# Optimization experiments

Hardware: AMD Instinct MI355X
Metric: run time of the kernel (lower is better)

Reference implementation:

```python
import jax, jax.numpy as jnp
import numpy as np

B, T, E, V, H = 4096, 80, 100, 10000, 64


def setup_inputs() -> dict:
    key = jax.random.key(0)
    ks = jax.random.split(key, 8)
    s = lambda k, sh: (jax.random.normal(k, sh, jnp.float32) * 0.05)
    return {
        "inputs": jax.random.randint(ks[0], (B, T), 0, V),
        "emb": s(ks[1], (V, E)),
        "Wx0": s(ks[2], (E, H)),
        "Wh0": s(ks[3], (H, H)),
        "b0": jnp.zeros((H,), jnp.float32),
        "Wx1": s(ks[4], (H, H)),
        "Wh1": s(ks[5], (H, H)),
        "b1": jnp.zeros((H,), jnp.float32),
        "Wf": s(ks[6], (H, 1)),
        "bf": jnp.zeros((1,), jnp.float32),
    }


def reference(inputs, emb, Wx0, Wh0, b0, Wx1, Wh1, b1, Wf, bf):
    # Embedding lookup: [B, T] int -> [B, T, E]
    x = emb[inputs]
    xT = jnp.swapaxes(x, 0, 1)  # [T, B, E] for scan over time

    def step(carry, xt):
        h0, h1 = carry
        # SimpleRNNCell layer 0: tanh(x@Wx + h@Wh + b)
        h0 = jnp.tanh(xt @ Wx0 + h0 @ Wh0 + b0)
        # SimpleRNNCell layer 1 consumes layer-0 output
        h1 = jnp.tanh(h0 @ Wx1 + h1 @ Wh1 + b1)
        return (h0, h1), None

    init = (jnp.zeros((B, H), x.dtype), jnp.zeros((B, H), x.dtype))
    (h0_last, h1_last), _ = jax.lax.scan(step, init, xT)
    # Dense(1) + sigmoid on last timestep's layer-1 hidden state
    return jax.nn.sigmoid(h1_last @ Wf + bf)  # [B, 1]
```

## Files before the change

kernel.cpp:

```cpp
#include <hip/hip_runtime.h>
#include <stdint.h>

#define BB 4096
#define TT 80
#define EE 100
#define VV 10000
#define HH 64

typedef float f32x4 __attribute__((ext_vector_type(4)));
typedef _Float16 f16x8 __attribute__((ext_vector_type(8)));

union AF { uint32_t u[4]; f16x8 v; _Float16 e[8]; };

__device__ __forceinline__ uint32_t pk_f16(float lo, float hi){
  uint32_t r;
  asm("v_cvt_pkrtz_f16_f32 %0, %1, %2" : "=v"(r) : "v"(lo), "v"(hi));
  return r;
}

__device__ __forceinline__ uint32_t tanh_pk(uint32_t x, uint32_t one, uint32_t c3){
  uint32_t r, x2;
  asm("v_pk_mul_f16 %0, %1, %1" : "=v"(x2) : "v"(x));
  asm("v_pk_fma_f16 %0, %1, %2, %3" : "=v"(x2) : "v"(x2), "v"(c3), "v"(one));
  asm("v_pk_mul_f16 %0, %1, %2" : "=v"(r) : "v"(x), "v"(x2));
  return r;
}

__device__ __forceinline__ f16x8 bfrag(const uint32_t P[4][2], int kk){
  AF r;
  r.u[0] = P[2*kk][0];   r.u[1] = P[2*kk][1];
  r.u[2] = P[2*kk+1][0]; r.u[3] = P[2*kk+1][1];
  return r.v;
}

__device__ __forceinline__ void tick_barrier(){
  asm volatile("s_waitcnt lgkmcnt(0)" ::: "memory");
  __builtin_amdgcn_s_barrier();
  asm volatile("" ::: "memory");
}

__global__ __launch_bounds__(64) void build_table_mfma(
    const float* __restrict__ emb, const float* __restrict__ Wx0,
    const float* __restrict__ b0, float* __restrict__ table){
  const int lane = threadIdx.x & 63;
  const int c = lane & 15, g = lane >> 4;
  const int v0 = blockIdx.x * 16;

  AF Aem[4];
  const float* er = emb + (v0 + c)*EE;
  #pragma unroll
  for (int kk = 0; kk < 4; kk++){
    #pragma unroll
    for (int p = 0; p < 4; p++){
      int k0 = 32*kk + 8*g + 2*p;
      int ks0 = (k0   < EE) ? k0   : 0;
      int ks1 = (k0+1 < EE) ? k0+1 : 0;
      float e0 = er[ks0]; if (k0   >= EE) e0 = 0.f;
      float e1 = er[ks1]; if (k0+1 >= EE) e1 = 0.f;
      Aem[kk].u[p] = pk_f16(e0, e1);
    }
  }
  AF Bw[4][4];
  #pragma unroll
  for (int qp = 0; qp < 4; qp++){
    #pragma unroll
    for (int kk = 0; kk < 4; kk++){
      #pragma unroll
      for (int p = 0; p < 4; p++){
        int k0 = 32*kk + 8*g + 2*p;
        int ks0 = (k0   < EE) ? k0   : 0;
        int ks1 = (k0+1 < EE) ? k0+1 : 0;
        float w0v = Wx0[ks0*HH + 16*qp + c]; if (k0   >= EE) w0v = 0.f;
        float w1v = Wx0[ks1*HH + 16*qp + c]; if (k0+1 >= EE) w1v = 0.f;
        Bw[qp][kk].u[p] = pk_f16(w0v, w1v);
      }
    }
  }
  f32x4 acc[4];
  #pragma unroll
  for (int qp = 0; qp < 4; qp++){
    float bv = b0[16*qp + c];
    acc[qp].x = bv; acc[qp].y = bv; acc[qp].z = bv; acc[qp].w = bv;
  }
  #pragma unroll
  for (int kk = 0; kk < 4; kk++)
    #pragma unroll
    for (int qp = 0; qp < 4; qp++)
      acc[qp] = __builtin_amdgcn_mfma_f32_16x16x32_f16(Aem[kk].v, Bw[qp][kk].v, acc[qp], 0, 0, 0);
  #pragma unroll
  for (int qp = 0; qp < 4; qp++)
    #pragma unroll
    for (int i = 0; i < 4; i++)
      table[(v0 + 4*g + i)*HH + 16*qp + c] = acc[qp][i];
}

__global__ __launch_bounds__(128, 1) void rnn_fused2(
    const int* __restrict__ inputs, const float* __restrict__ table,
    const float* __restrict__ Wh0, const float* __restrict__ Wx1,
    const float* __restrict__ Wh1, const float* __restrict__ b1,
    const float* __restrict__ Wf, const float* __restrict__ bfp,
    float* __restrict__ out)
{
  __shared__ uint32_t xch[2][2][64][8];
  const int tid = threadIdx.x;
  const int wid = tid >> 6;
  const int lane = tid & 63;
  const int c = lane & 15, g = lane >> 4;
  const int b0r = blockIdx.x * 16;

  const uint32_t one = 0x3C003C00u, c3 = 0xB555B555u;

  f32x4 b1c[4];
  #pragma unroll
  for (int q = 0; q < 4; q++) b1c[q] = *(const f32x4*)(b1 + 16*q + 4*g);

  if (wid == 0){
    AF A0[4][2], A1h[2][2];
    #pragma unroll
    for (int q = 0; q < 4; q++)
      #pragma unroll
      for (int kk = 0; kk < 2; kk++)
        #pragma unroll
        for (int p = 0; p < 4; p++){
          int hid = 32*kk + 16*(p>>1) + 4*g + 2*(p&1);
          int o0 = hid*HH + 16*q + c;
          A0[q][kk].u[p] = pk_f16(Wh0[o0], Wh0[o0+HH]);
        }
    #pragma unroll
    for (int q2 = 0; q2 < 2; q2++)
      #pragma unroll
      for (int kk = 0; kk < 2; kk++)
        #pragma unroll
        for (int p = 0; p < 4; p++){
          int hid = 32*kk + 16*(p>>1) + 4*g + 2*(p&1);
          int o0 = hid*HH + 16*q2 + c;
          A1h[q2][kk].u[p] = pk_f16(Wx1[o0], Wx1[o0+HH]);
        }

    uint32_t P0[4][2];
    #pragma unroll
    for (int q = 0; q < 4; q++){ P0[q][0] = 0u; P0[q][1] = 0u; }

    const int* ip = inputs + (b0r + c)*TT;
    int4 idxA = *(const int4*)(ip);
    int4 idxB = *(const int4*)(ip + 4);
    f32x4 zp[4][4];
    #pragma unroll
    for (int s = 0; s < 4; s++){
      int pidx = (s==0)?idxA.x:(s==1)?idxA.y:(s==2)?idxA.z:idxA.w;
      const float* tb = table + pidx*HH + 4*g;
      #pragma unroll
      for (int q = 0; q < 4; q++) zp[s][q] = *(const f32x4*)(tb + 16*q);
    }

    #pragma unroll 1
    for (int o = 0; o < 21; ++o){
      int tp = 4*o + 8; if (tp > TT-4) tp = TT-4;
      int4 idxC = *(const int4*)(ip + tp);
      #pragma unroll
      for (int s = 0; s < 4; ++s){
        if (4*o + s < TT){
          int pidx = (s==0)?idxB.x:(s==1)?idxB.y:(s==2)?idxB.z:idxB.w;
          f32x4 acc[4];
          #pragma unroll
          for (int q = 0; q < 4; q++)
            acc[q] = __builtin_amdgcn_mfma_f32_16x16x32_f16(A0[q][0].v, bfrag(P0,0), zp[s][q], 0, 0, 0);
          {
            const float* tb = table + pidx*HH + 4*g;
            #pragma unroll
            for (int q = 0; q < 4; q++) zp[s][q] = *(const f32x4*)(tb + 16*q);
          }
          #pragma unroll
          for (int q = 0; q < 4; q++)
            acc[q] = __builtin_amdgcn_mfma_f32_16x16x32_f16(A0[q][1].v, bfrag(P0,1), acc[q], 0, 0, 0);
          #pragma unroll
          for (int q = 0; q < 4; q++){
            P0[q][0] = tanh_pk(pk_f16(acc[q].x, acc[q].y), one, c3);
            P0[q][1] = tanh_pk(pk_f16(acc[q].z, acc[q].w), one, c3);
          }
          f32x4 pc0 = __builtin_amdgcn_mfma_f32_16x16x32_f16(A1h[0][0].v, bfrag(P0,0), b1c[0], 0, 0, 0);
          f32x4 pc1 = __builtin_amdgcn_mfma_f32_16x16x32_f16(A1h[1][0].v, bfrag(P0,0), b1c[1], 0, 0, 0);
          pc0 = __builtin_amdgcn_mfma_f32_16x16x32_f16(A1h[0][1].v, bfrag(P0,1), pc0, 0, 0, 0);
          pc1 = __builtin_amdgcn_mfma_f32_16x16x32_f16(A1h[1][1].v, bfrag(P0,1), pc1, 0, 0, 0);
          const int slot = s & 1;
          uint4 s0; s0.x=P0[0][0]; s0.y=P0[0][1]; s0.z=P0[1][0]; s0.w=P0[1][1];
          uint4 s1; s1.x=P0[2][0]; s1.y=P0[2][1]; s1.z=P0[3][0]; s1.w=P0[3][1];
          *(uint4*)&xch[slot][0][lane][0] = s0;
          *(uint4*)&xch[slot][0][lane][4] = s1;
          *(f32x4*)&xch[slot][1][lane][0] = pc0;
          *(f32x4*)&xch[slot][1][lane][4] = pc1;
        }
        tick_barrier();
      }
      idxB = idxC;
    }
  } else {
    AF A2[4][2], A1h[2][2];
    #pragma unroll
    for (int q = 0; q < 4; q++)
      #pragma unroll
      for (int kk = 0; kk < 2; kk++)
        #pragma unroll
        for (int p = 0; p < 4; p++){
          int hid = 32*kk + 16*(p>>1) + 4*g + 2*(p&1);
          int o0 = hid*HH + 16*q + c;
          A2[q][kk].u[p] = pk_f16(Wh1[o0], Wh1[o0+HH]);
        }
    #pragma unroll
    for (int q2 = 0; q2 < 2; q2++)
      #pragma unroll
      for (int kk = 0; kk < 2; kk++)
        #pragma unroll
        for (int p = 0; p < 4; p++){
          int hid = 32*kk + 16*(p>>1) + 4*g + 2*(p&1);
          int o0 = hid*HH + 16*(2+q2) + c;
          A1h[q2][kk].u[p] = pk_f16(Wx1[o0], Wx1[o0+HH]);
        }

    uint32_t P1[4][2];
    #pragma unroll
    for (int q = 0; q < 4; q++){ P1[q][0] = 0u; P1[q][1] = 0u; }

    #pragma unroll 1
    for (int o = 0; o < 21; ++o){
      #pragma unroll
      for (int s = 0; s < 4; ++s){
        int T = 4*o + s;
        if (T >= 1 && T <= TT){
          const int slot = (s + 1) & 1;
          AF bl0, bl1;
          *(uint4*)&bl0.u[0] = *(const uint4*)&xch[slot][0][lane][0];
          *(uint4*)&bl1.u[0] = *(const uint4*)&xch[slot][0][lane][4];
          f32x4 pc0 = *(const f32x4*)&xch[slot][1][lane][0];
          f32x4 pc1 = *(const f32x4*)&xch[slot][1][lane][4];
          f32x4 acc2 = __builtin_amdgcn_mfma_f32_16x16x32_f16(A2[2][0].v, bfrag(P1,0), b1c[2], 0, 0, 0);
          f32x4 acc3 = __builtin_amdgcn_mfma_f32_16x16x32_f16(A2[3][0].v, bfrag(P1,0), b1c[3], 0, 0, 0);
          acc2 = __builtin_amdgcn_mfma_f32_16x16x32_f16(A2[2][1].v, bfrag(P1,1), acc2, 0, 0, 0);
          acc3 = __builtin_amdgcn_mfma_f32_16x16x32_f16(A2[3][1].v, bfrag(P1,1), acc3, 0, 0, 0);
          f32x4 acc0 = __builtin_amdgcn_mfma_f32_16x16x32_f16(A2[0][0].v, bfrag(P1,0), pc0, 0, 0, 0);
          f32x4 acc1 = __builtin_amdgcn_mfma_f32_16x16x32_f16(A2[1][0].v, bfrag(P1,0), pc1, 0, 0, 0);
          acc0 = __builtin_amdgcn_mfma_f32_16x16x32_f16(A2[0][1].v, bfrag(P1,1), acc0, 0, 0, 0);
          acc1 = __builtin_amdgcn_mfma_f32_16x16x32_f16(A2[1][1].v, bfrag(P1,1), acc1, 0, 0, 0);
          acc2 = __builtin_amdgcn_mfma_f32_16x16x32_f16(A1h[0][0].v, bl0.v, acc2, 0, 0, 0);
          acc3 = __builtin_amdgcn_mfma_f32_16x16x32_f16(A1h[1][0].v, bl0.v, acc3, 0, 0, 0);
          acc2 = __builtin_amdgcn_mfma_f32_16x16x32_f16(A1h[0][1].v, bl1.v, acc2, 0, 0, 0);
          acc3 = __builtin_amdgcn_mfma_f32_16x16x32_f16(A1h[1][1].v, bl1.v, acc3, 0, 0, 0);
          P1[0][0] = tanh_pk(pk_f16(acc0.x, acc0.y), one, c3);
          P1[0][1] = tanh_pk(pk_f16(acc0.z, acc0.w), one, c3);
          P1[1][0] = tanh_pk(pk_f16(acc1.x, acc1.y), one, c3);
          P1[1][1] = tanh_pk(pk_f16(acc1.z, acc1.w), one, c3);
          P1[2][0] = tanh_pk(pk_f16(acc2.x, acc2.y), one, c3);
          P1[2][1] = tanh_pk(pk_f16(acc2.z, acc2.w), one, c3);
          P1[3][0] = tanh_pk(pk_f16(acc3.x, acc3.y), one, c3);
          P1[3][1] = tanh_pk(pk_f16(acc3.z, acc3.w), one, c3);
        }
        tick_barrier();
      }
    }

    float sv = 0.f;
    #pragma unroll
    for (int q = 0; q < 4; q++)
      #pragma unroll
      for (int p = 0; p < 2; p++){
        AF u; u.u[0] = P1[q][p];
        int hb = 16*q + 4*g + 2*p;
        sv = fmaf((float)u.e[0], Wf[hb],   sv);
        sv = fmaf((float)u.e[1], Wf[hb+1], sv);
      }
    sv += __shfl_xor(sv, 16, 64);
    sv += __shfl_xor(sv, 32, 64);
    sv += bfp[0];
    float r = 1.0f / (1.0f + __expf(-sv));
    if (lane < 16) out[b0r + lane] = r;
  }
}

extern "C" void kernel_launch(void* const* d_in, const int* in_sizes, int n_in,
                              void* d_out, int out_size, void* d_ws, size_t ws_size,
                              hipStream_t stream){
  const int*   inputs = (const int*)d_in[0];
  const float* emb = (const float*)d_in[1];
  const float* Wx0 = (const float*)d_in[2];
  const float* Wh0 = (const float*)d_in[3];
  const float* b0  = (const float*)d_in[4];
  const float* Wx1 = (const float*)d_in[5];
  const float* Wh1 = (const float*)d_in[6];
  const float* b1  = (const float*)d_in[7];
  const float* Wf  = (const float*)d_in[8];
  const float* bf  = (const float*)d_in[9];
  float* out   = (float*)d_out;
  float* table = (float*)d_ws;

  build_table_mfma<<<dim3(VV/16), dim3(64), 0, stream>>>(emb, Wx0, b0, table);
  rnn_fused2<<<dim3(BB/16), dim3(128), 0, stream>>>(inputs, table, Wh0, Wx1, Wh1, b1, Wf, bf, out);
}
```

Before: 41.48 us.

## Split RNN into three-wave pipeline with dedicated Wx1 projection wave

```diff
diff --git a/kernel.cpp b/kernel.cpp
--- a/kernel.cpp
+++ b/kernel.cpp
@@ -11,13 +11,13 @@
 typedef _Float16 f16x8 __attribute__((ext_vector_type(8)));
 
 union AF { uint32_t u[4]; f16x8 v; _Float16 e[8]; };
+union F4U { f32x4 f; uint2 u2[2]; };
 
 __device__ __forceinline__ uint32_t pk_f16(float lo, float hi){
   uint32_t r;
   asm("v_cvt_pkrtz_f16_f32 %0, %1, %2" : "=v"(r) : "v"(lo), "v"(hi));
   return r;
 }
-
 __device__ __forceinline__ uint32_t tanh_pk(uint32_t x, uint32_t one, uint32_t c3){
   uint32_t r, x2;
   asm("v_pk_mul_f16 %0, %1, %1" : "=v"(x2) : "v"(x));
@@ -25,19 +25,19 @@
   asm("v_pk_mul_f16 %0, %1, %2" : "=v"(r) : "v"(x), "v"(x2));
   return r;
 }
-
 __device__ __forceinline__ f16x8 bfrag(const uint32_t P[4][2], int kk){
   AF r;
   r.u[0] = P[2*kk][0];   r.u[1] = P[2*kk][1];
   r.u[2] = P[2*kk+1][0]; r.u[3] = P[2*kk+1][1];
   return r.v;
 }
-
 __device__ __forceinline__ void tick_barrier(){
   asm volatile("s_waitcnt lgkmcnt(0)" ::: "memory");
   __builtin_amdgcn_s_barrier();
   asm volatile("" ::: "memory");
 }
+
+#define MF(Af, Bf, Cf) __builtin_amdgcn_mfma_f32_16x16x32_f16((Af).v, (Bf), (Cf), 0, 0, 0)
 
 __global__ __launch_bounds__(64) void build_table_mfma(
     const float* __restrict__ emb, const float* __restrict__ Wx0,
@@ -94,28 +94,131 @@
       table[(v0 + 4*g + i)*HH + 16*qp + c] = acc[qp][i];
 }
 
-__global__ __launch_bounds__(128, 1) void rnn_fused2(
+#define L0STEP(S, SLOT, SU, PIDX) { \
+  f32x4 aA0 = MF(A0[0][0], bfrag(P0,0), zp[S][0]); \
+  f32x4 aA1 = MF(A0[1][0], bfrag(P0,0), zp[S][1]); \
+  f32x4 aA2 = MF(A0[2][0], bfrag(P0,0), zp[S][2]); \
+  f32x4 aA3 = MF(A0[3][0], bfrag(P0,0), zp[S][3]); \
+  f32x4 aB0 = MF(A0[0][1], bfrag(P0,1), kz); \
+  f32x4 aB1 = MF(A0[1][1], bfrag(P0,1), kz); \
+  f32x4 aB2 = MF(A0[2][1], bfrag(P0,1), kz); \
+  f32x4 aB3 = MF(A0[3][1], bfrag(P0,1), kz); \
+  { const float* tb_ = table + (PIDX)*HH + 4*g; \
+    zp[S][0] = *(const f32x4*)(tb_); \
+    zp[S][1] = *(const f32x4*)(tb_ + 16); \
+    zp[S][2] = *(const f32x4*)(tb_ + 32); \
+    zp[S][3] = *(const f32x4*)(tb_ + 48); } \
+  f32x4 ac0 = aA0 + aB0, ac1 = aA1 + aB1, ac2 = aA2 + aB2, ac3 = aA3 + aB3; \
+  P0[0][0] = tanh_pk(pk_f16(ac0.x, ac0.y), one, c3); P0[0][1] = tanh_pk(pk_f16(ac0.z, ac0.w), one, c3); \
+  P0[1][0] = tanh_pk(pk_f16(ac1.x, ac1.y), one, c3); P0[1][1] = tanh_pk(pk_f16(ac1.z, ac1.w), one, c3); \
+  P0[2][0] = tanh_pk(pk_f16(ac2.x, ac2.y), one, c3); P0[2][1] = tanh_pk(pk_f16(ac2.z, ac2.w), one, c3); \
+  P0[3][0] = tanh_pk(pk_f16(ac3.x, ac3.y), one, c3); P0[3][1] = tanh_pk(pk_f16(ac3.z, ac3.w), one, c3); \
+  xh0[SLOT][SU][0][lane] = make_uint2(P0[0][0], P0[0][1]); \
+  xh0[SLOT][SU][1][lane] = make_uint2(P0[1][0], P0[1][1]); \
+  xh0[SLOT][SU][2][lane] = make_uint2(P0[2][0], P0[2][1]); \
+  xh0[SLOT][SU][3][lane] = make_uint2(P0[3][0], P0[3][1]); \
+}
+
+#define PCTICK(RS, WS) { \
+  uint2 r00 = xh0[RS][0][0][lane], r01 = xh0[RS][0][1][lane]; \
+  uint2 r02 = xh0[RS][0][2][lane], r03 = xh0[RS][0][3][lane]; \
+  uint2 r10 = xh0[RS][1][0][lane], r11 = xh0[RS][1][1][lane]; \
+  uint2 r12 = xh0[RS][1][2][lane], r13 = xh0[RS][1][3][lane]; \
+  AF s0l0, s0l1, s1l0, s1l1; \
+  s0l0.u[0]=r00.x; s0l0.u[1]=r00.y; s0l0.u[2]=r01.x; s0l0.u[3]=r01.y; \
+  s0l1.u[0]=r02.x; s0l1.u[1]=r02.y; s0l1.u[2]=r03.x; s0l1.u[3]=r03.y; \
+  s1l0.u[0]=r10.x; s1l0.u[1]=r10.y; s1l0.u[2]=r11.x; s1l0.u[3]=r11.y; \
+  s1l1.u[0]=r12.x; s1l1.u[1]=r12.y; s1l1.u[2]=r13.x; s1l1.u[3]=r13.y; \
+  f32x4 p00 = MF(A1[0][0], s0l0.v, b1c[0]); \
+  f32x4 p01 = MF(A1[1][0], s0l0.v, b1c[1]); \
+  f32x4 p02 = MF(A1[2][0], s0l0.v, b1c[2]); \
+  f32x4 p03 = MF(A1[3][0], s0l0.v, b1c[3]); \
+  p00 = MF(A1[0][1], s0l1.v, p00); \
+  p01 = MF(A1[1][1], s0l1.v, p01); \
+  p02 = MF(A1[2][1], s0l1.v, p02); \
+  p03 = MF(A1[3][1], s0l1.v, p03); \
+  f32x4 p10 = MF(A1[0][0], s1l0.v, b1c[0]); \
+  f32x4 p11 = MF(A1[1][0], s1l0.v, b1c[1]); \
+  f32x4 p12 = MF(A1[2][0], s1l0.v, b1c[2]); \
+  f32x4 p13 = MF(A1[3][0], s1l0.v, b1c[3]); \
+  p10 = MF(A1[0][1], s1l1.v, p10); \
+  p11 = MF(A1[1][1], s1l1.v, p11); \
+  p12 = MF(A1[2][1], s1l1.v, p12); \
+  p13 = MF(A1[3][1], s1l1.v, p13); \
+  F4U tt; \
+  tt.f = p00; xpc[WS][0][0][lane] = tt.u2[0]; xpc[WS][0][1][lane] = tt.u2[1]; \
+  tt.f = p01; xpc[WS][0][2][lane] = tt.u2[0]; xpc[WS][0][3][lane] = tt.u2[1]; \
+  tt.f = p02; xpc[WS][0][4][lane] = tt.u2[0]; xpc[WS][0][5][lane] = tt.u2[1]; \
+  tt.f = p03; xpc[WS][0][6][lane] = tt.u2[0]; xpc[WS][0][7][lane] = tt.u2[1]; \
+  tt.f = p10; xpc[WS][1][0][lane] = tt.u2[0]; xpc[WS][1][1][lane] = tt.u2[1]; \
+  tt.f = p11; xpc[WS][1][2][lane] = tt.u2[0]; xpc[WS][1][3][lane] = tt.u2[1]; \
+  tt.f = p12; xpc[WS][1][4][lane] = tt.u2[0]; xpc[WS][1][5][lane] = tt.u2[1]; \
+  tt.f = p13; xpc[WS][1][6][lane] = tt.u2[0]; xpc[WS][1][7][lane] = tt.u2[1]; \
+}
+
+#define H1TICK(PS) { \
+  uint2 c00 = xpc[PS][0][0][lane], c01 = xpc[PS][0][1][lane]; \
+  uint2 c02 = xpc[PS][0][2][lane], c03 = xpc[PS][0][3][lane]; \
+  uint2 c04 = xpc[PS][0][4][lane], c05 = xpc[PS][0][5][lane]; \
+  uint2 c06 = xpc[PS][0][6][lane], c07 = xpc[PS][0][7][lane]; \
+  uint2 c10 = xpc[PS][1][0][lane], c11 = xpc[PS][1][1][lane]; \
+  uint2 c12 = xpc[PS][1][2][lane], c13 = xpc[PS][1][3][lane]; \
+  uint2 c14 = xpc[PS][1][4][lane], c15 = xpc[PS][1][5][lane]; \
+  uint2 c16 = xpc[PS][1][6][lane], c17 = xpc[PS][1][7][lane]; \
+  f32x4 wA0 = MF(A2[0][0], bfrag(P1,0), kz); \
+  f32x4 wA1 = MF(A2[1][0], bfrag(P1,0), kz); \
+  f32x4 wA2 = MF(A2[2][0], bfrag(P1,0), kz); \
+  f32x4 wA3 = MF(A2[3][0], bfrag(P1,0), kz); \
+  f32x4 wB0 = MF(A2[0][1], bfrag(P1,1), kz); \
+  f32x4 wB1 = MF(A2[1][1], bfrag(P1,1), kz); \
+  f32x4 wB2 = MF(A2[2][1], bfrag(P1,1), kz); \
+  f32x4 wB3 = MF(A2[3][1], bfrag(P1,1), kz); \
+  F4U q0, q1, q2, q3; \
+  q0.u2[0]=c00; q0.u2[1]=c01; q1.u2[0]=c02; q1.u2[1]=c03; \
+  q2.u2[0]=c04; q2.u2[1]=c05; q3.u2[0]=c06; q3.u2[1]=c07; \
+  f32x4 a0 = wA0 + wB0 + q0.f, a1 = wA1 + wB1 + q1.f; \
+  f32x4 a2 = wA2 + wB2 + q2.f, a3 = wA3 + wB3 + q3.f; \
+  P1[0][0] = tanh_pk(pk_f16(a0.x, a0.y), one, c3); P1[0][1] = tanh_pk(pk_f16(a0.z, a0.w), one, c3); \
+  P1[1][0] = tanh_pk(pk_f16(a1.x, a1.y), one, c3); P1[1][1] = tanh_pk(pk_f16(a1.z, a1.w), one, c3); \
+  P1[2][0] = tanh_pk(pk_f16(a2.x, a2.y), one, c3); P1[2][1] = tanh_pk(pk_f16(a2.z, a2.w), one, c3); \
+  P1[3][0] = tanh_pk(pk_f16(a3.x, a3.y), one, c3); P1[3][1] = tanh_pk(pk_f16(a3.z, a3.w), one, c3); \
+  f32x4 vA0 = MF(A2[0][0], bfrag(P1,0), kz); \
+  f32x4 vA1 = MF(A2[1][0], bfrag(P1,0), kz); \
+  f32x4 vA2 = MF(A2[2][0], bfrag(P1,0), kz); \
+  f32x4 vA3 = MF(A2[3][0], bfrag(P1,0), kz); \
+  f32x4 vB0 = MF(A2[0][1], bfrag(P1,1), kz); \
+  f32x4 vB1 = MF(A2[1][1], bfrag(P1,1), kz); \
+  f32x4 vB2 = MF(A2[2][1], bfrag(P1,1), kz); \
+  f32x4 vB3 = MF(A2[3][1], bfrag(P1,1), kz); \
+  q0.u2[0]=c10; q0.u2[1]=c11; q1.u2[0]=c12; q1.u2[1]=c13; \
+  q2.u2[0]=c14; q2.u2[1]=c15; q3.u2[0]=c16; q3.u2[1]=c17; \
+  f32x4 b0_ = vA0 + vB0 + q0.f, b1_ = vA1 + vB1 + q1.f; \
+  f32x4 b2_ = vA2 + vB2 + q2.f, b3_ = vA3 + vB3 + q3.f; \
+  P1[0][0] = tanh_pk(pk_f16(b0_.x, b0_.y), one, c3); P1[0][1] = tanh_pk(pk_f16(b0_.z, b0_.w), one, c3); \
+  P1[1][0] = tanh_pk(pk_f16(b1_.x, b1_.y), one, c3); P1[1][1] = tanh_pk(pk_f16(b1_.z, b1_.w), one, c3); \
+  P1[2][0] = tanh_pk(pk_f16(b2_.x, b2_.y), one, c3); P1[2][1] = tanh_pk(pk_f16(b2_.z, b2_.w), one, c3); \
+  P1[3][0] = tanh_pk(pk_f16(b3_.x, b3_.y), one, c3); P1[3][1] = tanh_pk(pk_f16(b3_.z, b3_.w), one, c3); \
+}
+
+__global__ __launch_bounds__(192, 1) void rnn_fused3(
     const int* __restrict__ inputs, const float* __restrict__ table,
     const float* __restrict__ Wh0, const float* __restrict__ Wx1,
     const float* __restrict__ Wh1, const float* __restrict__ b1,
     const float* __restrict__ Wf, const float* __restrict__ bfp,
     float* __restrict__ out)
 {
-  __shared__ uint32_t xch[2][2][64][8];
+  __shared__ uint2 xh0[2][2][4][64];
+  __shared__ uint2 xpc[2][2][8][64];
   const int tid = threadIdx.x;
   const int wid = tid >> 6;
   const int lane = tid & 63;
   const int c = lane & 15, g = lane >> 4;
   const int b0r = blockIdx.x * 16;
-
   const uint32_t one = 0x3C003C00u, c3 = 0xB555B555u;
-
-  f32x4 b1c[4];
-  #pragma unroll
-  for (int q = 0; q < 4; q++) b1c[q] = *(const f32x4*)(b1 + 16*q + 4*g);
+  const f32x4 kz = {0.f, 0.f, 0.f, 0.f};
 
   if (wid == 0){
-    AF A0[4][2], A1h[2][2];
+    AF A0[4][2];
     #pragma unroll
     for (int q = 0; q < 4; q++)
       #pragma unroll
@@ -126,76 +229,69 @@
           int o0 = hid*HH + 16*q + c;
           A0[q][kk].u[p] = pk_f16(Wh0[o0], Wh0[o0+HH]);
         }
-    #pragma unroll
-    for (int q2 = 0; q2 < 2; q2++)
+    uint32_t P0[4][2];
+    #pragma unroll
+    for (int q = 0; q < 4; q++){ P0[q][0] = 0u; P0[q][1] = 0u; }
+
+    const int* ip = inputs + (b0r + c)*TT;
+    int4 idxA = *(const int4*)(ip);
+    int4 idxB = *(const int4*)(ip + 4);
+    f32x4 zp[4][4];
+    {
+      const float* t0 = table + idxA.x*HH + 4*g;
+      const float* t1 = table + idxA.y*HH + 4*g;
+      const float* t2 = table + idxA.z*HH + 4*g;
+      const float* t3 = table + idxA.w*HH + 4*g;
+      #pragma unroll
+      for (int q = 0; q < 4; q++){
+        zp[0][q] = *(const f32x4*)(t0 + 16*q);
+        zp[1][q] = *(const f32x4*)(t1 + 16*q);
+        zp[2][q] = *(const f32x4*)(t2 + 16*q);
+        zp[3][q] = *(const f32x4*)(t3 + 16*q);
+      }
+    }
+    #pragma unroll 1
+    for (int om = 0; om <= 20; ++om){
+      int4 idxC;
+      if (om < 20){
+        int off = 4*om + 8; if (off > 76) off = 76;
+        idxC = *(const int4*)(ip + off);
+        L0STEP(0, 0, 0, idxB.x)
+        L0STEP(1, 0, 1, idxB.y)
+      }
+      tick_barrier();
+      if (om < 20){
+        L0STEP(2, 1, 0, idxB.z)
+        L0STEP(3, 1, 1, idxB.w)
+        idxB = idxC;
+      }
+      tick_barrier();
+    }
+  } else if (wid == 1){
+    AF A1[4][2];
+    #pragma unroll
+    for (int q = 0; q < 4; q++)
       #pragma unroll
       for (int kk = 0; kk < 2; kk++)
         #pragma unroll
         for (int p = 0; p < 4; p++){
           int hid = 32*kk + 16*(p>>1) + 4*g + 2*(p&1);
-          int o0 = hid*HH + 16*q2 + c;
-          A1h[q2][kk].u[p] = pk_f16(Wx1[o0], Wx1[o0+HH]);
+          int o0 = hid*HH + 16*q + c;
+          A1[q][kk].u[p] = pk_f16(Wx1[o0], Wx1[o0+HH]);
         }
-
-    uint32_t P0[4][2];
-    #pragma unroll
-    for (int q = 0; q < 4; q++){ P0[q][0] = 0u; P0[q][1] = 0u; }
-
-    const int* ip = inputs + (b0r + c)*TT;
-    int4 idxA = *(const int4*)(ip);
-    int4 idxB = *(const int4*)(ip + 4);
-    f32x4 zp[4][4];
-    #pragma unroll
-    for (int s = 0; s < 4; s++){
-      int pidx = (s==0)?idxA.x:(s==1)?idxA.y:(s==2)?idxA.z:idxA.w;
-      const float* tb = table + pidx*HH + 4*g;
-      #pragma unroll
-      for (int q = 0; q < 4; q++) zp[s][q] = *(const f32x4*)(tb + 16*q);
-    }
+    f32x4 b1c[4];
+    #pragma unroll
+    for (int q = 0; q < 4; q++) b1c[q] = *(const f32x4*)(b1 + 16*q + 4*g);
 
     #pragma unroll 1
-    for (int o = 0; o < 21; ++o){
-      int tp = 4*o + 8; if (tp > TT-4) tp = TT-4;
-      int4 idxC = *(const int4*)(ip + tp);
-      #pragma unroll
-      for (int s = 0; s < 4; ++s){
-        if (4*o + s < TT){
-          int pidx = (s==0)?idxB.x:(s==1)?idxB.y:(s==2)?idxB.z:idxB.w;
-          f32x4 acc[4];
-          #pragma unroll
-          for (int q = 0; q < 4; q++)
-            acc[q] = __builtin_amdgcn_mfma_f32_16x16x32_f16(A0[q][0].v, bfrag(P0,0), zp[s][q], 0, 0, 0);
-          {
-            const float* tb = table + pidx*HH + 4*g;
-            #pragma unroll
-            for (int q = 0; q < 4; q++) zp[s][q] = *(const f32x4*)(tb + 16*q);
-          }
-          #pragma unroll
-          for (int q = 0; q < 4; q++)
-            acc[q] = __builtin_amdgcn_mfma_f32_16x16x32_f16(A0[q][1].v, bfrag(P0,1), acc[q], 0, 0, 0);
-          #pragma unroll
-          for (int q = 0; q < 4; q++){
-            P0[q][0] = tanh_pk(pk_f16(acc[q].x, acc[q].y), one, c3);
-            P0[q][1] = tanh_pk(pk_f16(acc[q].z, acc[q].w), one, c3);
-          }
-          f32x4 pc0 = __builtin_amdgcn_mfma_f32_16x16x32_f16(A1h[0][0].v, bfrag(P0,0), b1c[0], 0, 0, 0);
-          f32x4 pc1 = __builtin_amdgcn_mfma_f32_16x16x32_f16(A1h[1][0].v, bfrag(P0,0), b1c[1], 0, 0, 0);
-          pc0 = __builtin_amdgcn_mfma_f32_16x16x32_f16(A1h[0][1].v, bfrag(P0,1), pc0, 0, 0, 0);
-          pc1 = __builtin_amdgcn_mfma_f32_16x16x32_f16(A1h[1][1].v, bfrag(P0,1), pc1, 0, 0, 0);
-          const int slot = s & 1;
-          uint4 s0; s0.x=P0[0][0]; s0.y=P0[0][1]; s0.z=P0[1][0]; s0.w=P0[1][1];
-          uint4 s1; s1.x=P0[2][0]; s1.y=P0[2][1]; s1.z=P0[3][0]; s1.w=P0[3][1];
-          *(uint4*)&xch[slot][0][lane][0] = s0;
-          *(uint4*)&xch[slot][0][lane][4] = s1;
-          *(f32x4*)&xch[slot][1][lane][0] = pc0;
-          *(f32x4*)&xch[slot][1][lane][4] = pc1;
-        }
-        tick_barrier();
-      }
-      idxB = idxC;
+    for (int om = 0; om <= 20; ++om){
+      if (om >= 1){ PCTICK(1, 0) }
+      tick_barrier();
+      if (om < 20){ PCTICK(0, 1) }
+      tick_barrier();
     }
   } else {
-    AF A2[4][2], A1h[2][2];
+    AF A2[4][2];
     #pragma unroll
     for (int q = 0; q < 4; q++)
       #pragma unroll
@@ -206,56 +302,16 @@
           int o0 = hid*HH + 16*q + c;
           A2[q][kk].u[p] = pk_f16(Wh1[o0], Wh1[o0+HH]);
         }
-    #pragma unroll
-    for (int q2 = 0; q2 < 2; q2++)
-      #pragma unroll
-      for (int kk = 0; kk < 2; kk++)
-        #pragma unroll
-        for (int p = 0; p < 4; p++){
-          int hid = 32*kk + 16*(p>>1) + 4*g + 2*(p&1);
-          int o0 = hid*HH + 16*(2+q2) + c;
-          A1h[q2][kk].u[p] = pk_f16(Wx1[o0], Wx1[o0+HH]);
-        }
-
     uint32_t P1[4][2];
     #pragma unroll
     for (int q = 0; q < 4; q++){ P1[q][0] = 0u; P1[q][1] = 0u; }
 
     #pragma unroll 1
-    for (int o = 0; o < 21; ++o){
-      #pragma unroll
-      for (int s = 0; s < 4; ++s){
-        int T = 4*o + s;
-        if (T >= 1 && T <= TT){
-          const int slot = (s + 1) & 1;
-          AF bl0, bl1;
-          *(uint4*)&bl0.u[0] = *(const uint4*)&xch[slot][0][lane][0];
-          *(uint4*)&bl1.u[0] = *(const uint4*)&xch[slot][0][lane][4];
-          f32x4 pc0 = *(const f32x4*)&xch[slot][1][lane][0];
-          f32x4 pc1 = *(const f32x4*)&xch[slot][1][lane][4];
-          f32x4 acc2 = __builtin_amdgcn_mfma_f32_16x16x32_f16(A2[2][0].v, bfrag(P1,0), b1c[2], 0, 0, 0);
-          f32x4 acc3 = __builtin_amdgcn_mfma_f32_16x16x32_f16(A2[3][0].v, bfrag(P1,0), b1c[3], 0, 0, 0);
-          acc2 = __builtin_amdgcn_mfma_f32_16x16x32_f16(A2[2][1].v, bfrag(P1,1), acc2, 0, 0, 0);
-          acc3 = __builtin_amdgcn_mfma_f32_16x16x32_f16(A2[3][1].v, bfrag(P1,1), acc3, 0, 0, 0);
-          f32x4 acc0 = __builtin_amdgcn_mfma_f32_16x16x32_f16(A2[0][0].v, bfrag(P1,0), pc0, 0, 0, 0);
-          f32x4 acc1 = __builtin_amdgcn_mfma_f32_16x16x32_f16(A2[1][0].v, bfrag(P1,0), pc1, 0, 0, 0);
-          acc0 = __builtin_amdgcn_mfma_f32_16x16x32_f16(A2[0][1].v, bfrag(P1,1), acc0, 0, 0, 0);
-          acc1 = __builtin_amdgcn_mfma_f32_16x16x32_f16(A2[1][1].v, bfrag(P1,1), acc1, 0, 0, 0);
-          acc2 = __builtin_amdgcn_mfma_f32_16x16x32_f16(A1h[0][0].v, bl0.v, acc2, 0, 0, 0);
-          acc3 = __builtin_amdgcn_mfma_f32_16x16x32_f16(A1h[1][0].v, bl0.v, acc3, 0, 0, 0);
-          acc2 = __builtin_amdgcn_mfma_f32_16x16x32_f16(A1h[0][1].v, bl1.v, acc2, 0, 0, 0);
-          acc3 = __builtin_amdgcn_mfma_f32_16x16x32_f16(A1h[1][1].v, bl1.v, acc3, 0, 0, 0);
-          P1[0][0] = tanh_pk(pk_f16(acc0.x, acc0.y), one, c3);
-          P1[0][1] = tanh_pk(pk_f16(acc0.z, acc0.w), one, c3);
-          P1[1][0] = tanh_pk(pk_f16(acc1.x, acc1.y), one, c3);
-          P1[1][1] = tanh_pk(pk_f16(acc1.z, acc1.w), one, c3);
-          P1[2][0] = tanh_pk(pk_f16(acc2.x, acc2.y), one, c3);
-          P1[2][1] = tanh_pk(pk_f16(acc2.z, acc2.w), one, c3);
-          P1[3][0] = tanh_pk(pk_f16(acc3.x, acc3.y), one, c3);
-          P1[3][1] = tanh_pk(pk_f16(acc3.z, acc3.w), one, c3);
-        }
-        tick_barrier();
-      }
+    for (int om = 0; om <= 20; ++om){
+      if (om >= 1){ H1TICK(1) }
+      tick_barrier();
+      if (om >= 1){ H1TICK(0) }
+      tick_barrier();
     }
 
     float sv = 0.f;
@@ -293,5 +349,5 @@
   float* table = (float*)d_ws;
 
   build_table_mfma<<<dim3(VV/16), dim3(64), 0, stream>>>(emb, Wx0, b0, table);
-  rnn_fused2<<<dim3(BB/16), dim3(128), 0, stream>>>(inputs, table, Wh0, Wx1, Wh1, b1, Wf, bf, out);
-}
+  rnn_fused3<<<dim3(BB/16), dim3(192), 0, stream>>>(inputs, table, Wh0, Wx1, Wh1, b1, Wf, bf, out);
+}
```

Result: faster. 40.24 us (-3.0%).

## Split RNN into three-wave pipeline with chunked LDS exchange every 8 steps

Applied to the files above, without the earlier changes.

```diff
diff --git a/kernel.cpp b/kernel.cpp
--- a/kernel.cpp
+++ b/kernel.cpp
@@ -11,13 +11,18 @@
 typedef _Float16 f16x8 __attribute__((ext_vector_type(8)));
 
 union AF { uint32_t u[4]; f16x8 v; _Float16 e[8]; };
+union PU { uint32_t u[8]; f16x8 f[2]; _Float16 e[16]; };
 
 __device__ __forceinline__ uint32_t pk_f16(float lo, float hi){
   uint32_t r;
   asm("v_cvt_pkrtz_f16_f32 %0, %1, %2" : "=v"(r) : "v"(lo), "v"(hi));
   return r;
 }
-
+__device__ __forceinline__ uint32_t pk_add(uint32_t a, uint32_t b){
+  uint32_t r;
+  asm("v_pk_add_f16 %0, %1, %2" : "=v"(r) : "v"(a), "v"(b));
+  return r;
+}
 __device__ __forceinline__ uint32_t tanh_pk(uint32_t x, uint32_t one, uint32_t c3){
   uint32_t r, x2;
   asm("v_pk_mul_f16 %0, %1, %1" : "=v"(x2) : "v"(x));
@@ -25,19 +30,14 @@
   asm("v_pk_mul_f16 %0, %1, %2" : "=v"(r) : "v"(x), "v"(x2));
   return r;
 }
-
-__device__ __forceinline__ f16x8 bfrag(const uint32_t P[4][2], int kk){
-  AF r;
-  r.u[0] = P[2*kk][0];   r.u[1] = P[2*kk][1];
-  r.u[2] = P[2*kk+1][0]; r.u[3] = P[2*kk+1][1];
-  return r.v;
-}
-
 __device__ __forceinline__ void tick_barrier(){
   asm volatile("s_waitcnt lgkmcnt(0)" ::: "memory");
   __builtin_amdgcn_s_barrier();
   asm volatile("" ::: "memory");
 }
+
+#define MF(Af, Bf, Cf) __builtin_amdgcn_mfma_f32_16x16x32_f16((Af).v, (Bf), (Cf), 0, 0, 0)
+#define I4C(v, s) ((s)==0?(v).x:(s)==1?(v).y:(s)==2?(v).z:(v).w)
 
 __global__ __launch_bounds__(64) void build_table_mfma(
     const float* __restrict__ emb, const float* __restrict__ Wx0,
@@ -94,28 +94,26 @@
       table[(v0 + 4*g + i)*HH + 16*qp + c] = acc[qp][i];
 }
 
-__global__ __launch_bounds__(128, 1) void rnn_fused2(
+__global__ __launch_bounds__(192, 1) void rnn_fused6(
     const int* __restrict__ inputs, const float* __restrict__ table,
     const float* __restrict__ Wh0, const float* __restrict__ Wx1,
     const float* __restrict__ Wh1, const float* __restrict__ b1,
     const float* __restrict__ Wf, const float* __restrict__ bfp,
     float* __restrict__ out)
 {
-  __shared__ uint32_t xch[2][2][64][8];
+  __shared__ uint2 LB[8192];
+  uint2* Hh = LB;
+  uint2* Pc = LB + 4096;
+
   const int tid = threadIdx.x;
   const int wid = tid >> 6;
   const int lane = tid & 63;
   const int c = lane & 15, g = lane >> 4;
   const int b0r = blockIdx.x * 16;
-
   const uint32_t one = 0x3C003C00u, c3 = 0xB555B555u;
 
-  f32x4 b1c[4];
-  #pragma unroll
-  for (int q = 0; q < 4; q++) b1c[q] = *(const f32x4*)(b1 + 16*q + 4*g);
-
   if (wid == 0){
-    AF A0[4][2], A1h[2][2];
+    AF A0[4][2];
     #pragma unroll
     for (int q = 0; q < 4; q++)
       #pragma unroll
@@ -126,76 +124,118 @@
           int o0 = hid*HH + 16*q + c;
           A0[q][kk].u[p] = pk_f16(Wh0[o0], Wh0[o0+HH]);
         }
-    #pragma unroll
-    for (int q2 = 0; q2 < 2; q2++)
+    PU P0;
+    #pragma unroll
+    for (int i = 0; i < 8; i++) P0.u[i] = 0u;
+
+    const char* tb = (const char*)table;
+    const char* ib = (const char*)inputs;
+    const uint32_t gb = (uint32_t)(g << 4);
+    const uint32_t ibase = (uint32_t)((b0r + c) * TT * 4);
+
+    f32x4 z[4][4];
+    int4 idxHi;
+    {
+      int4 iA = *(const int4*)(ib + ibase);
+      idxHi   = *(const int4*)(ib + ibase + 16);
+      #pragma unroll
+      for (int s = 0; s < 4; s++){
+        uint32_t vo = ((uint32_t)I4C(iA, s) << 8) | gb;
+        #pragma unroll
+        for (int q = 0; q < 4; q++) z[s][q] = *(const f32x4*)(tb + vo + 64*q);
+      }
+    }
+
+    #pragma unroll 1
+    for (int it = 0; it < 12; ++it){
+      if (it < 10){
+        int toff = 8*it + 8; if (toff > 72) toff = 72;
+        int4 nA = *(const int4*)(ib + ibase + (uint32_t)(toff*4));
+        int4 nB = *(const int4*)(ib + ibase + (uint32_t)(toff*4) + 16);
+        uint2* H = Hh + (it & 1)*2048;
+        #pragma unroll
+        for (int s = 0; s < 8; ++s){
+          const int zs = s & 3;
+          int idxv = (s < 4) ? I4C(idxHi, s) : I4C(nA, s-4);
+          f32x4 a0 = MF(A0[0][0], P0.f[0], z[zs][0]);
+          f32x4 a1 = MF(A0[1][0], P0.f[0], z[zs][1]);
+          f32x4 a2 = MF(A0[2][0], P0.f[0], z[zs][2]);
+          f32x4 a3 = MF(A0[3][0], P0.f[0], z[zs][3]);
+          { uint32_t vo = ((uint32_t)idxv << 8) | gb;
+            z[zs][0] = *(const f32x4*)(tb + vo);
+            z[zs][1] = *(const f32x4*)(tb + vo + 64);
+            z[zs][2] = *(const f32x4*)(tb + vo + 128);
+            z[zs][3] = *(const f32x4*)(tb + vo + 192); }
+          a0 = MF(A0[0][1], P0.f[1], a0);
+          a1 = MF(A0[1][1], P0.f[1], a1);
+          a2 = MF(A0[2][1], P0.f[1], a2);
+          a3 = MF(A0[3][1], P0.f[1], a3);
+          P0.u[0] = tanh_pk(pk_f16(a0.x, a0.y), one, c3);
+          P0.u[1] = tanh_pk(pk_f16(a0.z, a0.w), one, c3);
+          P0.u[2] = tanh_pk(pk_f16(a1.x, a1.y), one, c3);
+          P0.u[3] = tanh_pk(pk_f16(a1.z, a1.w), one, c3);
+          P0.u[4] = tanh_pk(pk_f16(a2.x, a2.y), one, c3);
+          P0.u[5] = tanh_pk(pk_f16(a2.z, a2.w), one, c3);
+          P0.u[6] = tanh_pk(pk_f16(a3.x, a3.y), one, c3);
+          P0.u[7] = tanh_pk(pk_f16(a3.z, a3.w), one, c3);
+          H[(s*4 + 0)*64 + lane] = make_uint2(P0.u[0], P0.u[1]);
+          H[(s*4 + 1)*64 + lane] = make_uint2(P0.u[2], P0.u[3]);
+          H[(s*4 + 2)*64 + lane] = make_uint2(P0.u[4], P0.u[5]);
+          H[(s*4 + 3)*64 + lane] = make_uint2(P0.u[6], P0.u[7]);
+        }
+        idxHi = nB;
+      }
+      tick_barrier();
+    }
+  } else if (wid == 1){
+    AF A1[4][2];
+    #pragma unroll
+    for (int q = 0; q < 4; q++)
       #pragma unroll
       for (int kk = 0; kk < 2; kk++)
         #pragma unroll
         for (int p = 0; p < 4; p++){
           int hid = 32*kk + 16*(p>>1) + 4*g + 2*(p&1);
-          int o0 = hid*HH + 16*q2 + c;
-          A1h[q2][kk].u[p] = pk_f16(Wx1[o0], Wx1[o0+HH]);
-        }
-
-    uint32_t P0[4][2];
-    #pragma unroll
-    for (int q = 0; q < 4; q++){ P0[q][0] = 0u; P0[q][1] = 0u; }
-
-    const int* ip = inputs + (b0r + c)*TT;
-    int4 idxA = *(const int4*)(ip);
-    int4 idxB = *(const int4*)(ip + 4);
-    f32x4 zp[4][4];
-    #pragma unroll
-    for (int s = 0; s < 4; s++){
-      int pidx = (s==0)?idxA.x:(s==1)?idxA.y:(s==2)?idxA.z:idxA.w;
-      const float* tb = table + pidx*HH + 4*g;
-      #pragma unroll
-      for (int q = 0; q < 4; q++) zp[s][q] = *(const f32x4*)(tb + 16*q);
-    }
+          int o0 = hid*HH + 16*q + c;
+          A1[q][kk].u[p] = pk_f16(Wx1[o0], Wx1[o0+HH]);
+        }
+    f32x4 b1c[4];
+    #pragma unroll
+    for (int q = 0; q < 4; q++) b1c[q] = *(const f32x4*)(b1 + 16*q + 4*g);
 
     #pragma unroll 1
-    for (int o = 0; o < 21; ++o){
-      int tp = 4*o + 8; if (tp > TT-4) tp = TT-4;
-      int4 idxC = *(const int4*)(ip + tp);
-      #pragma unroll
-      for (int s = 0; s < 4; ++s){
-        if (4*o + s < TT){
-          int pidx = (s==0)?idxB.x:(s==1)?idxB.y:(s==2)?idxB.z:idxB.w;
-          f32x4 acc[4];
-          #pragma unroll
-          for (int q = 0; q < 4; q++)
-            acc[q] = __builtin_amdgcn_mfma_f32_16x16x32_f16(A0[q][0].v, bfrag(P0,0), zp[s][q], 0, 0, 0);
-          {
-            const float* tb = table + pidx*HH + 4*g;
-            #pragma unroll
-            for (int q = 0; q < 4; q++) zp[s][q] = *(const f32x4*)(tb + 16*q);
-          }
-          #pragma unroll
-          for (int q = 0; q < 4; q++)
-            acc[q] = __builtin_amdgcn_mfma_f32_16x16x32_f16(A0[q][1].v, bfrag(P0,1), acc[q], 0, 0, 0);
-          #pragma unroll
-          for (int q = 0; q < 4; q++){
-            P0[q][0] = tanh_pk(pk_f16(acc[q].x, acc[q].y), one, c3);
-            P0[q][1] = tanh_pk(pk_f16(acc[q].z, acc[q].w), one, c3);
-          }
-          f32x4 pc0 = __builtin_amdgcn_mfma_f32_16x16x32_f16(A1h[0][0].v, bfrag(P0,0), b1c[0], 0, 0, 0);
-          f32x4 pc1 = __builtin_amdgcn_mfma_f32_16x16x32_f16(A1h[1][0].v, bfrag(P0,0), b1c[1], 0, 0, 0);
-          pc0 = __builtin_amdgcn_mfma_f32_16x16x32_f16(A1h[0][1].v, bfrag(P0,1), pc0, 0, 0, 0);
-          pc1 = __builtin_amdgcn_mfma_f32_16x16x32_f16(A1h[1][1].v, bfrag(P0,1), pc1, 0, 0, 0);
-          const int slot = s & 1;
-          uint4 s0; s0.x=P0[0][0]; s0.y=P0[0][1]; s0.z=P0[1][0]; s0.w=P0[1][1];
-          uint4 s1; s1.x=P0[2][0]; s1.y=P0[2][1]; s1.z=P0[3][0]; s1.w=P0[3][1];
-          *(uint4*)&xch[slot][0][lane][0] = s0;
-          *(uint4*)&xch[slot][0][lane][4] = s1;
-          *(f32x4*)&xch[slot][1][lane][0] = pc0;
-          *(f32x4*)&xch[slot][1][lane][4] = pc1;
-        }
-        tick_barrier();
-      }
-      idxB = idxC;
+    for (int it = 0; it < 12; ++it){
+      if (it >= 1 && it <= 10){
+        const int sl = (it - 1) & 1;
+        uint2* H  = Hh + sl*2048;
+        uint2* PW = Pc + sl*2048;
+        #pragma unroll
+        for (int s = 0; s < 8; ++s){
+          uint2 r0 = H[(s*4 + 0)*64 + lane];
+          uint2 r1 = H[(s*4 + 1)*64 + lane];
+          uint2 r2 = H[(s*4 + 2)*64 + lane];
+          uint2 r3 = H[(s*4 + 3)*64 + lane];
+          PU h;
+          h.u[0]=r0.x; h.u[1]=r0.y; h.u[2]=r1.x; h.u[3]=r1.y;
+          h.u[4]=r2.x; h.u[5]=r2.y; h.u[6]=r3.x; h.u[7]=r3.y;
+          f32x4 d0 = MF(A1[0][0], h.f[0], b1c[0]);
+          f32x4 d1 = MF(A1[1][0], h.f[0], b1c[1]);
+          f32x4 d2 = MF(A1[2][0], h.f[0], b1c[2]);
+          f32x4 d3 = MF(A1[3][0], h.f[0], b1c[3]);
+          d0 = MF(A1[0][1], h.f[1], d0);
+          d1 = MF(A1[1][1], h.f[1], d1);
+          d2 = MF(A1[2][1], h.f[1], d2);
+          d3 = MF(A1[3][1], h.f[1], d3);
+          PW[(s*4 + 0)*64 + lane] = make_uint2(pk_f16(d0.x, d0.y), pk_f16(d0.z, d0.w));
+          PW[(s*4 + 1)*64 + lane] = make_uint2(pk_f16(d1.x, d1.y), pk_f16(d1.z, d1.w));
+          PW[(s*4 + 2)*64 + lane] = make_uint2(pk_f16(d2.x, d2.y), pk_f16(d2.z, d2.w));
+          PW[(s*4 + 3)*64 + lane] = make_uint2(pk_f16(d3.x, d3.y), pk_f16(d3.z, d3.w));
+        }
+      }
+      tick_barrier();
     }
   } else {
-    AF A2[4][2], A1h[2][2];
+    AF A2[4][2];
     #pragma unroll
     for (int q = 0; q < 4; q++)
       #pragma unroll
@@ -206,56 +246,41 @@
           int o0 = hid*HH + 16*q + c;
           A2[q][kk].u[p] = pk_f16(Wh1[o0], Wh1[o0+HH]);
         }
-    #pragma unroll
-    for (int q2 = 0; q2 < 2; q2++)
-      #pragma unroll
-      for (int kk = 0; kk < 2; kk++)
-        #pragma unroll
-        for (int p = 0; p < 4; p++){
-          int hid = 32*kk + 16*(p>>1) + 4*g + 2*(p&1);
-          int o0 = hid*HH + 16*(2+q2) + c;
-          A1h[q2][kk].u[p] = pk_f16(Wx1[o0], Wx1[o0+HH]);
-        }
-
-    uint32_t P1[4][2];
-    #pragma unroll
-    for (int q = 0; q < 4; q++){ P1[q][0] = 0u; P1[q][1] = 0u; }
+    PU P1;
+    #pragma unroll
+    for (int i = 0; i < 8; i++) P1.u[i] = 0u;
+    const f32x4 kz = {0.f, 0.f, 0.f, 0.f};
 
     #pragma unroll 1
-    for (int o = 0; o < 21; ++o){
-      #pragma unroll
-      for (int s = 0; s < 4; ++s){
-        int T = 4*o + s;
-        if (T >= 1 && T <= TT){
-          const int slot = (s + 1) & 1;
-          AF bl0, bl1;
-          *(uint4*)&bl0.u[0] = *(const uint4*)&xch[slot][0][lane][0];
-          *(uint4*)&bl1.u[0] = *(const uint4*)&xch[slot][0][lane][4];
-          f32x4 pc0 = *(const f32x4*)&xch[slot][1][lane][0];
-          f32x4 pc1 = *(const f32x4*)&xch[slot][1][lane][4];
-          f32x4 acc2 = __builtin_amdgcn_mfma_f32_16x16x32_f16(A2[2][0].v, bfrag(P1,0), b1c[2], 0, 0, 0);
-          f32x4 acc3 = __builtin_amdgcn_mfma_f32_16x16x32_f16(A2[3][0].v, bfrag(P1,0), b1c[3], 0, 0, 0);
-          acc2 = __builtin_amdgcn_mfma_f32_16x16x32_f16(A2[2][1].v, bfrag(P1,1), acc2, 0, 0, 0);
-          acc3 = __builtin_amdgcn_mfma_f32_16x16x32_f16(A2[3][1].v, bfrag(P1,1), acc3, 0, 0, 0);
-          f32x4 acc0 = __builtin_amdgcn_mfma_f32_16x16x32_f16(A2[0][0].v, bfrag(P1,0), pc0, 0, 0, 0);
-          f32x4 acc1 = __builtin_amdgcn_mfma_f32_16x16x32_f16(A2[1][0].v, bfrag(P1,0), pc1, 0, 0, 0);
-          acc0 = __builtin_amdgcn_mfma_f32_16x16x32_f16(A2[0][1].v, bfrag(P1,1), acc0, 0, 0, 0);
-          acc1 = __builtin_amdgcn_mfma_f32_16x16x32_f16(A2[1][1].v, bfrag(P1,1), acc1, 0, 0, 0);
-          acc2 = __builtin_amdgcn_mfma_f32_16x16x32_f16(A1h[0][0].v, bl0.v, acc2, 0, 0, 0);
-          acc3 = __builtin_amdgcn_mfma_f32_16x16x32_f16(A1h[1][0].v, bl0.v, acc3, 0, 0, 0);
-          acc2 = __builtin_amdgcn_mfma_f32_16x16x32_f16(A1h[0][1].v, bl1.v, acc2, 0, 0, 0);
-          acc3 = __builtin_amdgcn_mfma_f32_16x16x32_f16(A1h[1][1].v, bl1.v, acc3, 0, 0, 0);
-          P1[0][0] = tanh_pk(pk_f16(acc0.x, acc0.y), one, c3);
-          P1[0][1] = tanh_pk(pk_f16(acc0.z, acc0.w), one, c3);
-          P1[1][0] = tanh_pk(pk_f16(acc1.x, acc1.y), one, c3);
-          P1[1][1] = tanh_pk(pk_f16(acc1.z, acc1.w), one, c3);
-          P1[2][0] = tanh_pk(pk_f16(acc2.x, acc2.y), one, c3);
-          P1[2][1] = tanh_pk(pk_f16(acc2.z, acc2.w), one, c3);
-          P1[3][0] = tanh_pk(pk_f16(acc3.x, acc3.y), one, c3);
-          P1[3][1] = tanh_pk(pk_f16(acc3.z, acc3.w), one, c3);
-        }
-        tick_barrier();
-      }
+    for (int it = 0; it < 12; ++it){
+      if (it >= 2){
+        const int sl = (it - 2) & 1;
+        uint2* PR = Pc + sl*2048;
+        #pragma unroll
+        for (int s = 0; s < 8; ++s){
+          uint2 q0 = PR[(s*4 + 0)*64 + lane];
+          uint2 q1 = PR[(s*4 + 1)*64 + lane];
+          uint2 q2 = PR[(s*4 + 2)*64 + lane];
+          uint2 q3 = PR[(s*4 + 3)*64 + lane];
+          f32x4 e0 = MF(A2[0][0], P1.f[0], kz);
+          f32x4 e1 = MF(A2[1][0], P1.f[0], kz);
+          f32x4 e2 = MF(A2[2][0], P1.f[0], kz);
+          f32x4 e3 = MF(A2[3][0], P1.f[0], kz);
+          e0 = MF(A2[0][1], P1.f[1], e0);
+          e1 = MF(A2[1][1], P1.f[1], e1);
+          e2 = MF(A2[2][1], P1.f[1], e2);
+          e3 = MF(A2[3][1], P1.f[1], e3);
+          P1.u[0] = tanh_pk(pk_add(pk_f16(e0.x, e0.y), q0.x), one, c3);
+          P1.u[1] = tanh_pk(pk_add(pk_f16(e0.z, e0.w), q0.y), one, c3);
+          P1.u[2] = tanh_pk(pk_add(pk_f16(e1.x, e1.y), q1.x), one, c3);
+          P1.u[3] = tanh_pk(pk_add(pk_f16(e1.z, e1.w), q1.y), one, c3);
+          P1.u[4] = tanh_pk(pk_add(pk_f16(e2.x, e2.y), q2.x), one, c3);
+          P1.u[5] = tanh_pk(pk_add(pk_f16(e2.z, e2.w), q2.y), one, c3);
+          P1.u[6] = tanh_pk(pk_add(pk_f16(e3.x, e3.y), q3.x), one, c3);
+          P1.u[7] = tanh_pk(pk_add(pk_f16(e3.z, e3.w), q3.y), one, c3);
+        }
+      }
+      tick_barrier();
     }
 
     float sv = 0.f;
@@ -263,7 +288,7 @@
     for (int q = 0; q < 4; q++)
       #pragma unroll
       for (int p = 0; p < 2; p++){
-        AF u; u.u[0] = P1[q][p];
+        AF u; u.u[0] = P1.u[2*q + p];
         int hb = 16*q + 4*g + 2*p;
         sv = fmaf((float)u.e[0], Wf[hb],   sv);
         sv = fmaf((float)u.e[1], Wf[hb+1], sv);
@@ -293,5 +318,5 @@
   float* table = (float*)d_ws;
 
   build_table_mfma<<<dim3(VV/16), dim3(64), 0, stream>>>(emb, Wx0, b0, table);
-  rnn_fused2<<<dim3(BB/16), dim3(128), 0, stream>>>(inputs, table, Wh0, Wx1, Wh1, b1, Wf, bf, out);
-}
+  rnn_fused6<<<dim3(BB/16), dim3(192), 0, stream>>>(inputs, table, Wh0, Wx1, Wh1, b1, Wf, bf, out);
+}
```

Measured after the change: 33.54 us (median of 2 runs). 19.1% less time.
